# Optimization experiments

Measured on AMD Instinct MI355X. Metric: run time of the kernel, lower is better.

## Reference

```python
import math
import jax, jax.numpy as jnp
import numpy as np

B, S, H = 4, 2048, 1024      # batch, seq_len, hidden_size
E, K, I = 8, 2, 1024         # n_routed_experts, top_k, expert intermediate
NSH = 2                      # n_shared_experts -> shared intermediate = NSH*I
CF, RSF = 1.25, 1.0          # capacity_factor, routed_scaling_factor


def setup_inputs() -> dict:
    key = jax.random.key(0)
    ks = jax.random.split(key, 8)
    w = lambda k, sh: jax.random.normal(k, sh, dtype=jnp.float32) * 0.02
    return {
        "hidden_states": jax.random.normal(ks[0], (B, S, H), dtype=jnp.float32),
        "gate_w":  w(ks[1], (E, H)),          # router weight (torch Linear layout)
        "we_gate": w(ks[2], (E, I, H)),       # per-expert gate_proj
        "we_up":   w(ks[3], (E, I, H)),       # per-expert up_proj
        "we_down": w(ks[4], (E, H, I)),       # per-expert down_proj
        "ws_gate": w(ks[5], (NSH * I, H)),    # shared expert gate_proj
        "ws_up":   w(ks[6], (NSH * I, H)),
        "ws_down": w(ks[7], (H, NSH * I)),
    }


def reference(hidden_states, gate_w, we_gate, we_up, we_down, ws_gate, ws_up, ws_down):
    orig_shape = hidden_states.shape
    x = hidden_states.reshape(-1, H)                       # [N, H]
    N = x.shape[0]

    # ---- gate (fp32 softmax + top-k, normalized, scaled) ----
    logits = x.astype(jnp.float32) @ gate_w.astype(jnp.float32).T   # [N, E]
    scores = jax.nn.softmax(logits, axis=-1)
    topk_w, topk_idx = jax.lax.top_k(scores, K)                      # [N, K]
    topk_w = topk_w / (topk_w.sum(-1, keepdims=True) + 1e-20) * RSF  # norm_topk_prob

    # ---- capacity masking: position of each (token,k) slot within its expert ----
    capacity = math.ceil(CF * N * K / E)
    flat = topk_idx.reshape(-1)                                      # [N*K]
    one_hot = jax.nn.one_hot(flat, E, dtype=jnp.int32)               # [N*K, E]
    pos = jnp.cumsum(one_hot, axis=0) - 1                            # running count per expert
    pos_tok = jnp.take_along_axis(pos, flat[:, None], axis=1)[:, 0]  # [N*K]
    keep = (pos_tok < capacity).reshape(N, K)
    topk_w = topk_w * keep.astype(topk_w.dtype)

    # ---- combine weights per (token, expert); dropped slots contribute 0 ----
    comb = jnp.zeros((N, E), jnp.float32).at[jnp.arange(N)[:, None], topk_idx].add(topk_w)

    # ---- routed experts: dense SwiGLU per expert, weighted combine ----
    g = jnp.einsum('nh,eih->nei', x, we_gate)                        # [N, E, I]
    u = jnp.einsum('nh,eih->nei', x, we_up)
    eo = jnp.einsum('nei,ehi->neh', jax.nn.silu(g) * u, we_down)     # [N, E, H]
    y = jnp.einsum('neh,ne->nh', eo, comb)                           # [N, H]

    # ---- shared experts ----
    sh = (jax.nn.silu(x @ ws_gate.T) * (x @ ws_up.T)) @ ws_down.T    # [N, H]

    return (y + sh).reshape(orig_shape)
```

## Files before the change

### kernel.cpp

```cpp
#include <hip/hip_runtime.h>

typedef unsigned short u16;

#define NTOK 8192
#define HD   1024
#define NEXP 8
#define CAP  2560

typedef __bf16 bf16x8 __attribute__((ext_vector_type(8)));
typedef float  f32x4  __attribute__((ext_vector_type(4)));

__device__ __forceinline__ u16 f2bf(float f){
  union { float f; unsigned u; } v; v.f = f;
  return (u16)((v.u + 0x7fffu + ((v.u >> 16) & 1u)) >> 16);
}
__device__ __forceinline__ float bf2f(u16 h){
  union { unsigned u; float f; } v; v.u = ((unsigned)h) << 16; return v.f;
}

__device__ __forceinline__ void async16(const void* g, void* l){
  __builtin_amdgcn_global_load_lds((__attribute__((address_space(1))) void*)(g),
                                   (__attribute__((address_space(3))) void*)(l), 16, 0, 0);
}

__global__ __launch_bounds__(256) void cast_kernel(const float* __restrict__ src,
                                                   u16* __restrict__ dst, int n4){
  int i = blockIdx.x * 256 + threadIdx.x;
  if (i >= n4) return;
  float4 v = ((const float4*)src)[i];
  ushort4 o;
  o.x = f2bf(v.x); o.y = f2bf(v.y); o.z = f2bf(v.z); o.w = f2bf(v.w);
  ((ushort4*)dst)[i] = o;
}

__global__ __launch_bounds__(256) void router_kernel(const float* __restrict__ x,
                                                     const float* __restrict__ gate_w,
                                                     int* __restrict__ topk_idx,
                                                     float* __restrict__ topk_w){
  __shared__ float gw[NEXP * HD];
  int t = threadIdx.x;
  for (int i = t; i < NEXP * HD; i += 256) gw[i] = gate_w[i];
  __syncthreads();
  int wave = t >> 6, l = t & 63;
  int tok = blockIdx.x * 4 + wave;
  const float* xr = x + (size_t)tok * HD;
  double acc[NEXP];
#pragma unroll
  for (int e = 0; e < NEXP; e++) acc[e] = 0.0;
  for (int j = 0; j < 16; j++){
    int h = j * 64 + l;
    double xv = (double)xr[h];
#pragma unroll
    for (int e = 0; e < NEXP; e++) acc[e] += xv * (double)gw[e * HD + h];
  }
#pragma unroll
  for (int e = 0; e < NEXP; e++){
    double v = acc[e];
#pragma unroll
    for (int off = 32; off > 0; off >>= 1) v += __shfl_down(v, off, 64);
    acc[e] = v;
  }
  if (l == 0){
    int i0 = 0; double l0 = acc[0];
#pragma unroll
    for (int e = 1; e < NEXP; e++) if (acc[e] > l0){ l0 = acc[e]; i0 = e; }
    int i1 = -1; double l1 = -1e300;
#pragma unroll
    for (int e = 0; e < NEXP; e++) if (e != i0 && acc[e] > l1){ l1 = acc[e]; i1 = e; }
    double e1 = exp(l1 - l0);
    double s  = 1.0 + e1;
    topk_idx[tok * 2 + 0] = i0;
    topk_idx[tok * 2 + 1] = i1;
    topk_w [tok * 2 + 0] = (float)(1.0 / s);
    topk_w [tok * 2 + 1] = (float)(e1 / s);
  }
}

__global__ __launch_bounds__(256) void scan_kernel(const int* __restrict__ topk_idx,
                                                   const float* __restrict__ topk_w,
                                                   int* __restrict__ tok_list,
                                                   float* __restrict__ w_list,
                                                   int* __restrict__ slot_map,
                                                   int* __restrict__ ne){
  __shared__ int hist[256][NEXP];
  int t = threadIdx.x;
  const int SPT = (NTOK * 2) / 256;
  int cnt[NEXP];
#pragma unroll
  for (int e = 0; e < NEXP; e++) cnt[e] = 0;
  int base = t * SPT;
  for (int s = 0; s < SPT; s++) cnt[topk_idx[base + s]]++;
#pragma unroll
  for (int e = 0; e < NEXP; e++) hist[t][e] = cnt[e];
  __syncthreads();
  if (t < NEXP){
    int run = 0;
    for (int i = 0; i < 256; i++){ int v = hist[i][t]; hist[i][t] = run; run += v; }
    ne[t] = run < CAP ? run : CAP;
  }
  __syncthreads();
  int pos[NEXP];
#pragma unroll
  for (int e = 0; e < NEXP; e++) pos[e] = hist[t][e];
  for (int s = 0; s < SPT; s++){
    int slot = base + s;
    int e = topk_idx[slot];
    int p = pos[e]++;
    if (p < CAP){
      tok_list[e * CAP + p] = slot >> 1;
      w_list [e * CAP + p] = topk_w[slot];
      slot_map[slot] = e * CAP + p;
    } else {
      slot_map[slot] = -1;
    }
  }
}

#define MODE_GU    0
#define MODE_WBF   1
#define MODE_FINAL 2

template<int MODE, int IND>
__global__ __launch_bounds__(256)
void gemm_bt(const u16* __restrict__ A, long long sAe,
             const u16* __restrict__ B0, const u16* __restrict__ B1, long long sBe,
             void* __restrict__ Cv, long long sCe, int ldc,
             const int* __restrict__ tok_list, const float* __restrict__ w_list,
             const int* __restrict__ ne,
             const u16* __restrict__ Ebuf, const int* __restrict__ slot_map,
             int M, int K)
{
  __shared__ u16 As[128 * 64];
  __shared__ u16 Bs[128 * 64];

  const int e  = blockIdx.z;
  const int m0 = blockIdx.y * 128;
  const int n0 = blockIdx.x * ((MODE == MODE_GU) ? 64 : 128);

  int n_valid = (IND || MODE == MODE_WBF) ? ne[e] : M;
  if (m0 >= n_valid) return;

  const u16* Ae = A + (size_t)e * sAe;
  const int* tl = tok_list + e * CAP;

  const int tid = threadIdx.x;
  const int wv  = tid >> 6;
  const int l   = tid & 63;
  const int lr  = l >> 3;
  const int cb  = (l & 7) ^ lr;

  const u16* aptr[4];
  const u16* bptr[4];
#pragma unroll
  for (int i = 0; i < 4; i++){
    int chunk = i * 4 + wv;
    int arow  = m0 + chunk * 8 + lr;
    if (IND){
      int r2 = arow < n_valid ? arow : (n_valid - 1);
      aptr[i] = Ae + (size_t)tl[r2] * K + cb * 8;
    } else {
      aptr[i] = Ae + (size_t)arow * K + cb * 8;
    }
    int rn = chunk * 8 + lr;
    if (MODE == MODE_GU){
      int w  = rn >> 6;
      int jq = (rn >> 4) & 3;
      int rl = rn & 15;
      int icol = n0 + w * 32 + (jq & 1) * 16 + rl;
      const u16* src = (jq < 2) ? B0 : B1;
      bptr[i] = src + (size_t)e * sBe + (size_t)icol * K + cb * 8;
    } else {
      bptr[i] = B0 + (size_t)e * sBe + (size_t)(n0 + rn) * K + cb * 8;
    }
  }

  const int wm = wv & 1, wn = wv >> 1;
  const int col = l & 15, quad = l >> 4;
  const int rr = col & 7, ch = col >> 3;

  f32x4 acc[4][4];
#pragma unroll
  for (int i = 0; i < 4; i++)
#pragma unroll
    for (int j = 0; j < 4; j++)
      acc[i][j] = (f32x4){0.f, 0.f, 0.f, 0.f};

  for (int k0 = 0; k0 < K; k0 += 64){
#pragma unroll
    for (int i = 0; i < 4; i++){
      int chunk = i * 4 + wv;
      async16(aptr[i] + k0, &As[chunk * 512 + l * 8]);
      async16(bptr[i] + k0, &Bs[chunk * 512 + l * 8]);
    }
    __syncthreads();
#pragma unroll
    for (int s = 0; s < 2; s++){
      const int so = (rr * 8 + ((quad + s * 4) ^ rr)) * 8;
      bf16x8 a[4], b[4];
#pragma unroll
      for (int i = 0; i < 4; i++) a[i] = *(const bf16x8*)&As[(wm * 8 + i * 2 + ch) * 512 + so];
#pragma unroll
      for (int j = 0; j < 4; j++) b[j] = *(const bf16x8*)&Bs[(wn * 8 + j * 2 + ch) * 512 + so];
#pragma unroll
      for (int i = 0; i < 4; i++)
#pragma unroll
        for (int j = 0; j < 4; j++)
          acc[i][j] = __builtin_amdgcn_mfma_f32_16x16x32_bf16(a[i], b[j], acc[i][j], 0, 0, 0);
    }
    __syncthreads();
  }

  if (MODE == MODE_GU){
    u16* C = (u16*)Cv + (size_t)e * sCe;
#pragma unroll
    for (int i = 0; i < 4; i++)
#pragma unroll
      for (int r = 0; r < 4; r++){
        int row = m0 + wm * 64 + i * 16 + quad * 4 + r;
#pragma unroll
        for (int j = 0; j < 2; j++){
          int cg = n0 + wn * 32 + j * 16 + col;
          float g = acc[i][j][r], u = acc[i][j + 2][r];
          float h = (g / (1.f + __expf(-g))) * u;
          C[(size_t)row * ldc + cg] = f2bf(h);
        }
      }
  } else if (MODE == MODE_WBF){
    u16* C = (u16*)Cv + (size_t)e * sCe;
    const float* wl = w_list + e * CAP;
#pragma unroll
    for (int i = 0; i < 4; i++)
#pragma unroll
      for (int r = 0; r < 4; r++){
        int row = m0 + wm * 64 + i * 16 + quad * 4 + r;
        if (row < n_valid){
          float wgt = wl[row];
#pragma unroll
          for (int j = 0; j < 4; j++){
            int cg = n0 + wn * 64 + j * 16 + col;
            C[(size_t)row * ldc + cg] = f2bf(wgt * acc[i][j][r]);
          }
        }
      }
  } else {
    float* C = (float*)Cv;
#pragma unroll
    for (int i = 0; i < 4; i++)
#pragma unroll
      for (int r = 0; r < 4; r++){
        int row = m0 + wm * 64 + i * 16 + quad * 4 + r;
        int s0 = slot_map[row * 2 + 0];
        int s1 = slot_map[row * 2 + 1];
#pragma unroll
        for (int j = 0; j < 4; j++){
          int cg = n0 + wn * 64 + j * 16 + col;
          float v = acc[i][j][r];
          if (s0 >= 0) v += bf2f(Ebuf[(size_t)s0 * HD + cg]);
          if (s1 >= 0) v += bf2f(Ebuf[(size_t)s1 * HD + cg]);
          C[(size_t)row * HD + cg] = v;
        }
      }
  }
}

extern "C" void kernel_launch(void* const* d_in, const int* in_sizes, int n_in,
                              void* d_out, int out_size, void* d_ws, size_t ws_size,
                              hipStream_t stream){
  const float* x       = (const float*)d_in[0];
  const float* gate_w  = (const float*)d_in[1];
  const float* we_gate = (const float*)d_in[2];
  const float* we_up   = (const float*)d_in[3];
  const float* we_down = (const float*)d_in[4];
  const float* ws_gate = (const float*)d_in[5];
  const float* ws_up   = (const float*)d_in[6];
  const float* ws_down = (const float*)d_in[7];
  float* out = (float*)d_out;

  char* p = (char*)d_ws;
  u16* x_bf   = (u16*)p; p += (size_t)NTOK * HD * 2;
  u16* wg_bf  = (u16*)p; p += (size_t)NEXP * 1024 * 1024 * 2;
  u16* wu_bf  = (u16*)p; p += (size_t)NEXP * 1024 * 1024 * 2;
  u16* wd_bf  = (u16*)p; p += (size_t)NEXP * 1024 * 1024 * 2;
  u16* wsg_bf = (u16*)p; p += (size_t)2048 * 1024 * 2;
  u16* wsu_bf = (u16*)p; p += (size_t)2048 * 1024 * 2;
  u16* wsd_bf = (u16*)p; p += (size_t)1024 * 2048 * 2;
  u16* Hbuf   = (u16*)p; p += (size_t)NEXP * CAP * 1024 * 2;
  u16* Ebuf   = (u16*)p; p += (size_t)NEXP * CAP * 1024 * 2;
  int*   topk_idx = (int*)p;   p += (size_t)NTOK * 2 * 4;
  float* topk_w   = (float*)p; p += (size_t)NTOK * 2 * 4;
  int*   tok_list = (int*)p;   p += (size_t)NEXP * CAP * 4;
  float* w_list   = (float*)p; p += (size_t)NEXP * CAP * 4;
  int*   slot_map = (int*)p;   p += (size_t)NTOK * 2 * 4;
  int*   ne       = (int*)p;   p += 128;

  auto cast = [&](const float* s, u16* d, size_t n){
    int n4 = (int)(n / 4);
    cast_kernel<<<dim3((n4 + 255) / 256), dim3(256), 0, stream>>>(s, d, n4);
  };
  cast(x,       x_bf,   (size_t)NTOK * HD);
  cast(we_gate, wg_bf,  (size_t)NEXP * 1024 * 1024);
  cast(we_up,   wu_bf,  (size_t)NEXP * 1024 * 1024);
  cast(we_down, wd_bf,  (size_t)NEXP * 1024 * 1024);
  cast(ws_gate, wsg_bf, (size_t)2048 * 1024);
  cast(ws_up,   wsu_bf, (size_t)2048 * 1024);
  cast(ws_down, wsd_bf, (size_t)1024 * 2048);

  router_kernel<<<dim3(NTOK / 4), dim3(256), 0, stream>>>(x, gate_w, topk_idx, topk_w);
  scan_kernel<<<dim3(1), dim3(256), 0, stream>>>(topk_idx, topk_w, tok_list, w_list, slot_map, ne);

  const long long WEXP = 1024LL * 1024;
  const long long SLOT = (long long)CAP * 1024;

  gemm_bt<MODE_GU, 1><<<dim3(16, 20, 8), 256, 0, stream>>>(
      x_bf, 0, wg_bf, wu_bf, WEXP, Hbuf, SLOT, 1024,
      tok_list, w_list, ne, nullptr, nullptr, CAP, 1024);
  gemm_bt<MODE_WBF, 0><<<dim3(8, 20, 8), 256, 0, stream>>>(
      Hbuf, SLOT, wd_bf, nullptr, WEXP, Ebuf, SLOT, 1024,
      tok_list, w_list, ne, nullptr, nullptr, CAP, 1024);

  gemm_bt<MODE_GU, 0><<<dim3(32, 64, 1), 256, 0, stream>>>(
      x_bf, 0, wsg_bf, wsu_bf, 0, Hbuf, 0, 2048,
      tok_list, w_list, ne, nullptr, nullptr, 8192, 1024);
  gemm_bt<MODE_FINAL, 0><<<dim3(8, 64, 1), 256, 0, stream>>>(
      Hbuf, 0, wsd_bf, nullptr, 0, out, 0, 1024,
      tok_list, w_list, ne, Ebuf, slot_map, 8192, 2048);
}
```

Measured before the change: 589.0 us.

## Merge casts with router and batch routed and shared gate/up GEMMs into one launch

The seven cast kernels and the router are fused into a single prep kernel that splits work by block index. The routed-expert and shared-expert gate/up GEMMs become one gu_kernel launch with a flat grid, so the two GEMMs fill the GPU together instead of running back to back. Separate H buffers are used for routed and shared outputs, and Ebuf now reuses the wg_bf region. This cuts launch overhead and tail underutilisation, at the cost of branchy block dispatch and less flexible buffer aliasing.

```diff
diff --git a/kernel.cpp b/kernel.cpp
--- a/kernel.cpp
+++ b/kernel.cpp
@@ -23,56 +23,69 @@
                                    (__attribute__((address_space(3))) void*)(l), 16, 0, 0);
 }
 
-__global__ __launch_bounds__(256) void cast_kernel(const float* __restrict__ src,
-                                                   u16* __restrict__ dst, int n4){
-  int i = blockIdx.x * 256 + threadIdx.x;
-  if (i >= n4) return;
-  float4 v = ((const float4*)src)[i];
-  ushort4 o;
-  o.x = f2bf(v.x); o.y = f2bf(v.y); o.z = f2bf(v.z); o.w = f2bf(v.w);
-  ((ushort4*)dst)[i] = o;
-}
-
-__global__ __launch_bounds__(256) void router_kernel(const float* __restrict__ x,
-                                                     const float* __restrict__ gate_w,
-                                                     int* __restrict__ topk_idx,
-                                                     float* __restrict__ topk_w){
+__global__ __launch_bounds__(256)
+void prep_kernel(const float* __restrict__ x, const float* __restrict__ gate_w,
+                 const float* __restrict__ we_gate, const float* __restrict__ we_up,
+                 const float* __restrict__ we_down, const float* __restrict__ ws_gate,
+                 const float* __restrict__ ws_up, const float* __restrict__ ws_down,
+                 u16* __restrict__ x_bf, u16* __restrict__ wg_bf, u16* __restrict__ wu_bf,
+                 u16* __restrict__ wd_bf, u16* __restrict__ wsg_bf, u16* __restrict__ wsu_bf,
+                 u16* __restrict__ wsd_bf,
+                 int* __restrict__ topk_idx, float* __restrict__ topk_w){
   __shared__ float gw[NEXP * HD];
+  int bid = blockIdx.x;
   int t = threadIdx.x;
-  for (int i = t; i < NEXP * HD; i += 256) gw[i] = gate_w[i];
-  __syncthreads();
-  int wave = t >> 6, l = t & 63;
-  int tok = blockIdx.x * 4 + wave;
-  const float* xr = x + (size_t)tok * HD;
-  double acc[NEXP];
-#pragma unroll
-  for (int e = 0; e < NEXP; e++) acc[e] = 0.0;
-  for (int j = 0; j < 16; j++){
-    int h = j * 64 + l;
-    double xv = (double)xr[h];
-#pragma unroll
-    for (int e = 0; e < NEXP; e++) acc[e] += xv * (double)gw[e * HD + h];
-  }
-#pragma unroll
-  for (int e = 0; e < NEXP; e++){
-    double v = acc[e];
-#pragma unroll
-    for (int off = 32; off > 0; off >>= 1) v += __shfl_down(v, off, 64);
-    acc[e] = v;
-  }
-  if (l == 0){
-    int i0 = 0; double l0 = acc[0];
-#pragma unroll
-    for (int e = 1; e < NEXP; e++) if (acc[e] > l0){ l0 = acc[e]; i0 = e; }
-    int i1 = -1; double l1 = -1e300;
-#pragma unroll
-    for (int e = 0; e < NEXP; e++) if (e != i0 && acc[e] > l1){ l1 = acc[e]; i1 = e; }
-    double e1 = exp(l1 - l0);
-    double s  = 1.0 + e1;
-    topk_idx[tok * 2 + 0] = i0;
-    topk_idx[tok * 2 + 1] = i1;
-    topk_w [tok * 2 + 0] = (float)(1.0 / s);
-    topk_w [tok * 2 + 1] = (float)(e1 / s);
+  if (bid < 2048){
+    for (int i = t; i < NEXP * HD; i += 256) gw[i] = gate_w[i];
+    __syncthreads();
+    int wave = t >> 6, l = t & 63;
+    int tok = bid * 4 + wave;
+    const float* xr = x + (size_t)tok * HD;
+    double acc[NEXP];
+#pragma unroll
+    for (int e = 0; e < NEXP; e++) acc[e] = 0.0;
+    for (int j = 0; j < 16; j++){
+      int h = j * 64 + l;
+      double xv = (double)xr[h];
+#pragma unroll
+      for (int e = 0; e < NEXP; e++) acc[e] += xv * (double)gw[e * HD + h];
+    }
+#pragma unroll
+    for (int e = 0; e < NEXP; e++){
+      double v = acc[e];
+#pragma unroll
+      for (int off = 32; off > 0; off >>= 1) v += __shfl_down(v, off, 64);
+      acc[e] = v;
+    }
+    if (l == 0){
+      int i0 = 0; double l0 = acc[0];
+#pragma unroll
+      for (int e = 1; e < NEXP; e++) if (acc[e] > l0){ l0 = acc[e]; i0 = e; }
+      int i1 = -1; double l1 = -1e300;
+#pragma unroll
+      for (int e = 0; e < NEXP; e++) if (e != i0 && acc[e] > l1){ l1 = acc[e]; i1 = e; }
+      double e1 = exp(l1 - l0);
+      double s  = 1.0 + e1;
+      topk_idx[tok * 2 + 0] = i0;
+      topk_idx[tok * 2 + 1] = i1;
+      topk_w [tok * 2 + 0] = (float)(1.0 / s);
+      topk_w [tok * 2 + 1] = (float)(e1 / s);
+    }
+  } else {
+    long long g = (long long)(bid - 2048) * 256 + t;
+    const float4* s; ushort4* d; long long off;
+    if      (g <  2097152){ s = (const float4*)x;       d = (ushort4*)x_bf;   off = 0; }
+    else if (g <  4194304){ s = (const float4*)we_gate; d = (ushort4*)wg_bf;  off = 2097152; }
+    else if (g <  6291456){ s = (const float4*)we_up;   d = (ushort4*)wu_bf;  off = 4194304; }
+    else if (g <  8388608){ s = (const float4*)we_down; d = (ushort4*)wd_bf;  off = 6291456; }
+    else if (g <  8912896){ s = (const float4*)ws_gate; d = (ushort4*)wsg_bf; off = 8388608; }
+    else if (g <  9437184){ s = (const float4*)ws_up;   d = (ushort4*)wsu_bf; off = 8912896; }
+    else                  { s = (const float4*)ws_down; d = (ushort4*)wsd_bf; off = 9437184; }
+    long long i = g - off;
+    float4 v = s[i];
+    ushort4 o;
+    o.x = f2bf(v.x); o.y = f2bf(v.y); o.z = f2bf(v.z); o.w = f2bf(v.w);
+    d[i] = o;
   }
 }
 
@@ -116,17 +129,124 @@
   }
 }
 
-#define MODE_GU    0
+__global__ __launch_bounds__(256)
+void gu_kernel(const u16* __restrict__ x_bf,
+               const u16* __restrict__ wg, const u16* __restrict__ wu,
+               const u16* __restrict__ wsg, const u16* __restrict__ wsu,
+               u16* __restrict__ Hr, u16* __restrict__ Hs,
+               const int* __restrict__ tok_list, const int* __restrict__ ne)
+{
+  __shared__ u16 As[128 * 64];
+  __shared__ u16 Bs[128 * 64];
+
+  const int bid = blockIdx.x;
+  const bool routed = bid < 2560;
+  int m0, n0, ldc, n_valid;
+  const u16 *B0, *B1;
+  u16* C;
+  const int* tl = nullptr;
+  if (routed){
+    int e = bid / 320, r = bid % 320;
+    m0 = (r / 16) * 128; n0 = (r % 16) * 64;
+    B0 = wg + (size_t)e * (1024 * 1024);
+    B1 = wu + (size_t)e * (1024 * 1024);
+    C  = Hr + (size_t)e * (CAP * 1024);
+    ldc = 1024;
+    n_valid = ne[e];
+    tl = tok_list + e * CAP;
+    if (m0 >= n_valid) return;
+  } else {
+    int b2 = bid - 2560;
+    n0 = (b2 / 64) * 64; m0 = (b2 % 64) * 128;
+    B0 = wsg; B1 = wsu; C = Hs; ldc = 2048; n_valid = 1 << 30;
+  }
+
+  const int tid = threadIdx.x;
+  const int wv  = tid >> 6;
+  const int l   = tid & 63;
+  const int lr  = l >> 3;
+  const int cb  = (l & 7) ^ lr;
+
+  const u16* aptr[4];
+  const u16* bptr[4];
+#pragma unroll
+  for (int i = 0; i < 4; i++){
+    int chunk = i * 4 + wv;
+    int arow  = m0 + chunk * 8 + lr;
+    if (routed){
+      int r2 = arow < n_valid ? arow : (n_valid - 1);
+      aptr[i] = x_bf + (size_t)tl[r2] * 1024 + cb * 8;
+    } else {
+      aptr[i] = x_bf + (size_t)arow * 1024 + cb * 8;
+    }
+    int rn = chunk * 8 + lr;
+    int w  = rn >> 6;
+    int jq = (rn >> 4) & 3;
+    int rl = rn & 15;
+    int icol = n0 + w * 32 + (jq & 1) * 16 + rl;
+    bptr[i] = ((jq < 2) ? B0 : B1) + (size_t)icol * 1024 + cb * 8;
+  }
+
+  const int wm = wv & 1, wn = wv >> 1;
+  const int col = l & 15, quad = l >> 4;
+  const int rr = col & 7, ch = col >> 3;
+
+  f32x4 acc[4][4];
+#pragma unroll
+  for (int i = 0; i < 4; i++)
+#pragma unroll
+    for (int j = 0; j < 4; j++)
+      acc[i][j] = (f32x4){0.f, 0.f, 0.f, 0.f};
+
+  for (int k0 = 0; k0 < 1024; k0 += 64){
+#pragma unroll
+    for (int i = 0; i < 4; i++){
+      int chunk = i * 4 + wv;
+      async16(aptr[i] + k0, &As[chunk * 512 + l * 8]);
+      async16(bptr[i] + k0, &Bs[chunk * 512 + l * 8]);
+    }
+    __syncthreads();
+#pragma unroll
+    for (int s = 0; s < 2; s++){
+      const int so = (rr * 8 + ((quad + s * 4) ^ rr)) * 8;
+      bf16x8 a[4], b[4];
+#pragma unroll
+      for (int i = 0; i < 4; i++) a[i] = *(const bf16x8*)&As[(wm * 8 + i * 2 + ch) * 512 + so];
+#pragma unroll
+      for (int j = 0; j < 4; j++) b[j] = *(const bf16x8*)&Bs[(wn * 8 + j * 2 + ch) * 512 + so];
+#pragma unroll
+      for (int i = 0; i < 4; i++)
+#pragma unroll
+        for (int j = 0; j < 4; j++)
+          acc[i][j] = __builtin_amdgcn_mfma_f32_16x16x32_bf16(a[i], b[j], acc[i][j], 0, 0, 0);
+    }
+    __syncthreads();
+  }
+
+#pragma unroll
+  for (int i = 0; i < 4; i++)
+#pragma unroll
+    for (int r = 0; r < 4; r++){
+      int row = m0 + wm * 64 + i * 16 + quad * 4 + r;
+#pragma unroll
+      for (int j = 0; j < 2; j++){
+        int cg = n0 + wn * 32 + j * 16 + col;
+        float g = acc[i][j][r], u = acc[i][j + 2][r];
+        float h = (g / (1.f + __expf(-g))) * u;
+        C[(size_t)row * ldc + cg] = f2bf(h);
+      }
+    }
+}
+
 #define MODE_WBF   1
 #define MODE_FINAL 2
 
-template<int MODE, int IND>
+template<int MODE>
 __global__ __launch_bounds__(256)
 void gemm_bt(const u16* __restrict__ A, long long sAe,
-             const u16* __restrict__ B0, const u16* __restrict__ B1, long long sBe,
+             const u16* __restrict__ B0, long long sBe,
              void* __restrict__ Cv, long long sCe, int ldc,
-             const int* __restrict__ tok_list, const float* __restrict__ w_list,
-             const int* __restrict__ ne,
+             const float* __restrict__ w_list, const int* __restrict__ ne,
              const u16* __restrict__ Ebuf, const int* __restrict__ slot_map,
              int M, int K)
 {
@@ -135,13 +255,12 @@
 
   const int e  = blockIdx.z;
   const int m0 = blockIdx.y * 128;
-  const int n0 = blockIdx.x * ((MODE == MODE_GU) ? 64 : 128);
-
-  int n_valid = (IND || MODE == MODE_WBF) ? ne[e] : M;
+  const int n0 = blockIdx.x * 128;
+
+  int n_valid = (MODE == MODE_WBF) ? ne[e] : M;
   if (m0 >= n_valid) return;
 
   const u16* Ae = A + (size_t)e * sAe;
-  const int* tl = tok_list + e * CAP;
 
   const int tid = threadIdx.x;
   const int wv  = tid >> 6;
@@ -155,23 +274,9 @@
   for (int i = 0; i < 4; i++){
     int chunk = i * 4 + wv;
     int arow  = m0 + chunk * 8 + lr;
-    if (IND){
-      int r2 = arow < n_valid ? arow : (n_valid - 1);
-      aptr[i] = Ae + (size_t)tl[r2] * K + cb * 8;
-    } else {
-      aptr[i] = Ae + (size_t)arow * K + cb * 8;
-    }
-    int rn = chunk * 8 + lr;
-    if (MODE == MODE_GU){
-      int w  = rn >> 6;
-      int jq = (rn >> 4) & 3;
-      int rl = rn & 15;
-      int icol = n0 + w * 32 + (jq & 1) * 16 + rl;
-      const u16* src = (jq < 2) ? B0 : B1;
-      bptr[i] = src + (size_t)e * sBe + (size_t)icol * K + cb * 8;
-    } else {
-      bptr[i] = B0 + (size_t)e * sBe + (size_t)(n0 + rn) * K + cb * 8;
-    }
+    aptr[i] = Ae + (size_t)arow * K + cb * 8;
+    int brow = n0 + chunk * 8 + lr;
+    bptr[i] = B0 + (size_t)e * sBe + (size_t)brow * K + cb * 8;
   }
 
   const int wm = wv & 1, wn = wv >> 1;
@@ -210,22 +315,7 @@
     __syncthreads();
   }
 
-  if (MODE == MODE_GU){
-    u16* C = (u16*)Cv + (size_t)e * sCe;
-#pragma unroll
-    for (int i = 0; i < 4; i++)
-#pragma unroll
-      for (int r = 0; r < 4; r++){
-        int row = m0 + wm * 64 + i * 16 + quad * 4 + r;
-#pragma unroll
-        for (int j = 0; j < 2; j++){
-          int cg = n0 + wn * 32 + j * 16 + col;
-          float g = acc[i][j][r], u = acc[i][j + 2][r];
-          float h = (g / (1.f + __expf(-g))) * u;
-          C[(size_t)row * ldc + cg] = f2bf(h);
-        }
-      }
-  } else if (MODE == MODE_WBF){
+  if (MODE == MODE_WBF){
     u16* C = (u16*)Cv + (size_t)e * sCe;
     const float* wl = w_list + e * CAP;
 #pragma unroll
@@ -280,48 +370,37 @@
   u16* x_bf   = (u16*)p; p += (size_t)NTOK * HD * 2;
   u16* wg_bf  = (u16*)p; p += (size_t)NEXP * 1024 * 1024 * 2;
   u16* wu_bf  = (u16*)p; p += (size_t)NEXP * 1024 * 1024 * 2;
-  u16* wd_bf  = (u16*)p; p += (size_t)NEXP * 1024 * 1024 * 2;
   u16* wsg_bf = (u16*)p; p += (size_t)2048 * 1024 * 2;
   u16* wsu_bf = (u16*)p; p += (size_t)2048 * 1024 * 2;
+  u16* wd_bf  = (u16*)p; p += (size_t)NEXP * 1024 * 1024 * 2;
   u16* wsd_bf = (u16*)p; p += (size_t)1024 * 2048 * 2;
-  u16* Hbuf   = (u16*)p; p += (size_t)NEXP * CAP * 1024 * 2;
-  u16* Ebuf   = (u16*)p; p += (size_t)NEXP * CAP * 1024 * 2;
+  u16* Hr     = (u16*)p; p += (size_t)NEXP * CAP * 1024 * 2;
+  u16* Hs     = (u16*)p; p += (size_t)NTOK * 2048 * 2;
   int*   topk_idx = (int*)p;   p += (size_t)NTOK * 2 * 4;
   float* topk_w   = (float*)p; p += (size_t)NTOK * 2 * 4;
   int*   tok_list = (int*)p;   p += (size_t)NEXP * CAP * 4;
   float* w_list   = (float*)p; p += (size_t)NEXP * CAP * 4;
   int*   slot_map = (int*)p;   p += (size_t)NTOK * 2 * 4;
   int*   ne       = (int*)p;   p += 128;
-
-  auto cast = [&](const float* s, u16* d, size_t n){
-    int n4 = (int)(n / 4);
-    cast_kernel<<<dim3((n4 + 255) / 256), dim3(256), 0, stream>>>(s, d, n4);
-  };
-  cast(x,       x_bf,   (size_t)NTOK * HD);
-  cast(we_gate, wg_bf,  (size_t)NEXP * 1024 * 1024);
-  cast(we_up,   wu_bf,  (size_t)NEXP * 1024 * 1024);
-  cast(we_down, wd_bf,  (size_t)NEXP * 1024 * 1024);
-  cast(ws_gate, wsg_bf, (size_t)2048 * 1024);
-  cast(ws_up,   wsu_bf, (size_t)2048 * 1024);
-  cast(ws_down, wsd_bf, (size_t)1024 * 2048);
-
-  router_kernel<<<dim3(NTOK / 4), dim3(256), 0, stream>>>(x, gate_w, topk_idx, topk_w);
+  u16* Ebuf = wg_bf;
+
+  prep_kernel<<<dim3(40960), dim3(256), 0, stream>>>(
+      x, gate_w, we_gate, we_up, we_down, ws_gate, ws_up, ws_down,
+      x_bf, wg_bf, wu_bf, wd_bf, wsg_bf, wsu_bf, wsd_bf, topk_idx, topk_w);
+
   scan_kernel<<<dim3(1), dim3(256), 0, stream>>>(topk_idx, topk_w, tok_list, w_list, slot_map, ne);
+
+  gu_kernel<<<dim3(4608), dim3(256), 0, stream>>>(
+      x_bf, wg_bf, wu_bf, wsg_bf, wsu_bf, Hr, Hs, tok_list, ne);
 
   const long long WEXP = 1024LL * 1024;
   const long long SLOT = (long long)CAP * 1024;
 
-  gemm_bt<MODE_GU, 1><<<dim3(16, 20, 8), 256, 0, stream>>>(
-      x_bf, 0, wg_bf, wu_bf, WEXP, Hbuf, SLOT, 1024,
-      tok_list, w_list, ne, nullptr, nullptr, CAP, 1024);
-  gemm_bt<MODE_WBF, 0><<<dim3(8, 20, 8), 256, 0, stream>>>(
-      Hbuf, SLOT, wd_bf, nullptr, WEXP, Ebuf, SLOT, 1024,
-      tok_list, w_list, ne, nullptr, nullptr, CAP, 1024);
-
-  gemm_bt<MODE_GU, 0><<<dim3(32, 64, 1), 256, 0, stream>>>(
-      x_bf, 0, wsg_bf, wsu_bf, 0, Hbuf, 0, 2048,
-      tok_list, w_list, ne, nullptr, nullptr, 8192, 1024);
-  gemm_bt<MODE_FINAL, 0><<<dim3(8, 64, 1), 256, 0, stream>>>(
-      Hbuf, 0, wsd_bf, nullptr, 0, out, 0, 1024,
-      tok_list, w_list, ne, Ebuf, slot_map, 8192, 2048);
-}
+  gemm_bt<MODE_WBF><<<dim3(8, 20, 8), 256, 0, stream>>>(
+      Hr, SLOT, wd_bf, WEXP, Ebuf, SLOT, 1024,
+      w_list, ne, nullptr, nullptr, CAP, 1024);
+
+  gemm_bt<MODE_FINAL><<<dim3(8, 64, 1), 256, 0, stream>>>(
+      Hs, 0, wsd_bf, 0, out, 0, 1024,
+      w_list, ne, Ebuf, slot_map, NTOK, 2048);
+}
```

Result: faster. 555.7 us (-5.7%).
